# Performance work log

Measured on AMD Instinct MI355X. Metric: run time of the kernel, lower is better.

The kernel has to match this reference:

```python
import jax, jax.numpy as jnp
import numpy as np

B, N, F_IN = 16, 2048, 64   # batch, node_num, input_dim
D = 64                      # dim == embed_dim == GNN out_channel
TOPK = 30
EPS = 1e-5
NEG_SLOPE = 0.2


def setup_inputs() -> dict:
    key = jax.random.key(0)
    k = jax.random.split(key, 20)
    u = lambda kk, shp, b: jax.random.uniform(kk, shp, jnp.float32, -b, b)
    return {
        "data": jax.random.normal(k[0], (B, N, F_IN), jnp.float32),
        "org_edge_index": jax.random.randint(k[1], (2, N * TOPK), 0, N),  # accepted but unused (prior_graph=True)
        "embedding_weight": u(k[2], (N, D), 1.0 / np.sqrt(D)),            # kaiming_uniform(a=sqrt(5)) bound
        "lin_w": u(k[3], (F_IN, D), 1.0 / np.sqrt(F_IN)),
        "att_i": jax.random.normal(k[4], (D,), jnp.float32) * 0.1,
        "att_j": jax.random.normal(k[5], (D,), jnp.float32) * 0.1,
        "att_em_i": jax.random.normal(k[6], (D,), jnp.float32) * 0.1,
        "att_em_j": jax.random.normal(k[7], (D,), jnp.float32) * 0.1,
        "gnn_bias": jax.random.normal(k[8], (D,), jnp.float32) * 0.01,
        "bn1_gamma": jax.random.uniform(k[9], (D,), jnp.float32, 0.5, 1.5),
        "bn1_beta": jax.random.normal(k[10], (D,), jnp.float32) * 0.1,
        "bn1_mean": jax.random.normal(k[11], (D,), jnp.float32) * 0.1,
        "bn1_var": jax.random.uniform(k[12], (D,), jnp.float32, 0.5, 1.5),
        "bn2_gamma": jax.random.uniform(k[13], (D,), jnp.float32, 0.5, 1.5),
        "bn2_beta": jax.random.normal(k[14], (D,), jnp.float32) * 0.1,
        "bn2_mean": jax.random.normal(k[15], (D,), jnp.float32) * 0.1,
        "bn2_var": jax.random.uniform(k[16], (D,), jnp.float32, 0.5, 1.5),
        "out_w": u(k[17], (D, 1), 1.0 / np.sqrt(D)),
        "out_b": jnp.zeros((1,), jnp.float32),
    }


def _forward(data, org_edge_index, embedding_weight, lin_w, att_i, att_j,
             att_em_i, att_em_j, gnn_bias,
             bn1_gamma, bn1_beta, bn1_mean, bn1_var,
             bn2_gamma, bn2_beta, bn2_mean, bn2_var,
             out_w, out_b):
    b, n, f = data.shape
    x = jax.lax.stop_gradient(data).reshape(b * n, f)  # torch: x = data.clone().detach()

    # --- dynamic graph: top-k cosine similarity over DETACHED embeddings ---
    w = jax.lax.stop_gradient(embedding_weight)        # weights_arr = embedding.detach().clone()
    nrm = jnp.linalg.norm(w, axis=-1, keepdims=True)
    cos = (w @ w.T) / (nrm * nrm.T)                    # [N, N]
    _, topk_idx = jax.lax.top_k(cos, TOPK)             # [N, k]; row i contains i itself (cos(i,i)=1 is the max),
                                                       # so remove_self_loops + add_self_loops leaves the edge set unchanged
    # batched sources; target of edge (i, kk) is node i -> each node receives exactly TOPK edges
    src = (topk_idx[None] + (jnp.arange(b) * n)[:, None, None]).reshape(b * n, TOPK)

    # --- GraphLayer (GAT-style, heads=1, concat=False -> mean over 1 head) ---
    xl = x @ lin_w                                     # [BN, D]
    emb_all = jnp.tile(embedding_weight, (b, 1))       # [BN, D] embeddings repeated per batch
    a_i = xl @ att_i + emb_all @ att_em_i              # per-node target score [BN]
    a_j = xl @ att_j + emb_all @ att_em_j              # per-node source score [BN]
    alpha = jax.nn.leaky_relu(a_i[:, None] + a_j[src], NEG_SLOPE)  # [BN, k]
    alpha = jax.nn.softmax(alpha, axis=-1)             # softmax over incoming edges per target node
    out = jnp.einsum('ek,ekd->ed', alpha, xl[src]) + gnn_bias      # per-edge gather + weighted add-aggregate

    # GNNLayer: BatchNorm1d (eval) + ReLU
    out = (out - bn1_mean) / jnp.sqrt(bn1_var + EPS) * bn1_gamma + bn1_beta
    out = jax.nn.relu(out)

    # --- readout ---
    h = out.reshape(b, n, D) * embedding_weight[None]  # elementwise mul with node embeddings
    h = (h - bn2_mean) / jnp.sqrt(bn2_var + EPS) * bn2_gamma + bn2_beta  # bn_outlayer_in (eval)
    h = jax.nn.relu(h)                                 # dropout = identity (eval)
    y = h @ out_w + out_b                              # OutLayer: single Linear(D, 1)
    return y.reshape(-1, n)                            # [B, N]


def reference(data, org_edge_index, embedding_weight, lin_w, att_i, att_j,
              att_em_i, att_em_j, gnn_bias,
              bn1_gamma, bn1_beta, bn1_mean, bn1_var,
              bn2_gamma, bn2_beta, bn2_mean, bn2_var,
              out_w, out_b):
    return _forward(data, org_edge_index, embedding_weight, lin_w, att_i, att_j,
                    att_em_i, att_em_j, gnn_bias,
                    bn1_gamma, bn1_beta, bn1_mean, bn1_var,
                    bn2_gamma, bn2_beta, bn2_mean, bn2_var,
                    out_w, out_b)
```

## Files before the change

kernel.cpp:

```cpp
#include <hip/hip_runtime.h>
#include <hip/hip_bf16.h>

#define NODES 2048
#define DIM   64
#define K_TOP 30
#define BATCH 16
#define BN    (NODES * BATCH)
#define NEGINF (-3.402823466e38f)
#define EPS 1e-5f
#define TB 64

template <int CTRL>
__device__ __forceinline__ float dpp_add_f32(float x) {
    int y = __builtin_amdgcn_update_dpp(0, __float_as_int(x), CTRL, 0xf, 0xf, true);
    return x + __int_as_float(y);
}

__device__ __forceinline__ float wave_sum(float x) {
    x = dpp_add_f32<0x111>(x);
    x = dpp_add_f32<0x112>(x);
    x = dpp_add_f32<0x114>(x);
    x = dpp_add_f32<0x118>(x);
    x = dpp_add_f32<0x142>(x);
    x = dpp_add_f32<0x143>(x);
    return __int_as_float(__builtin_amdgcn_readlane(__float_as_int(x), 63));
}

template <int CTRL>
__device__ __forceinline__ float dpp_max_f32(float x) {
    int y = __builtin_amdgcn_update_dpp(__float_as_int(x), __float_as_int(x),
                                        CTRL, 0xf, 0xf, false);
    return fmaxf(x, __int_as_float(y));
}

__device__ __forceinline__ float wave_max(float x) {
    x = dpp_max_f32<0x111>(x);
    x = dpp_max_f32<0x112>(x);
    x = dpp_max_f32<0x114>(x);
    x = dpp_max_f32<0x118>(x);
    x = dpp_max_f32<0x142>(x);
    x = dpp_max_f32<0x143>(x);
    return __int_as_float(__builtin_amdgcn_readlane(__float_as_int(x), 63));
}

#define ARGMAX_STEP(CTRL)                                                       \
    do {                                                                        \
        int nv_ = __builtin_amdgcn_update_dpp(__float_as_int(bv),               \
                      __float_as_int(bv), (CTRL), 0xf, 0xf, false);             \
        int nj_ = __builtin_amdgcn_update_dpp(bj, bj, (CTRL), 0xf, 0xf, false); \
        float nvf_ = __int_as_float(nv_);                                       \
        bool g_ = (nvf_ > bv) || (nvf_ == bv && nj_ < bj);                      \
        bv = g_ ? nvf_ : bv;                                                    \
        bj = g_ ? nj_ : bj;                                                     \
    } while (0)

#define TOP3_INSERT(x, j)                                                        \
    do {                                                                         \
        if ((x) > m1)      { m3 = m2; j3 = j2; m2 = m1; j2 = j1; m1 = (x); j1 = (j); } \
        else if ((x) > m2) { m3 = m2; j3 = j2; m2 = (x); j2 = (j); }             \
        else if ((x) > m3) { m3 = (x); j3 = (j); }                               \
    } while (0)

__global__ __launch_bounds__(256) void normalize_kernel(const float* __restrict__ w,
                                                        float* __restrict__ wn) {
    int r = blockIdx.x * 4 + (threadIdx.x >> 6);
    int lane = threadIdx.x & 63;
    float v = w[r * DIM + lane];
    float s = wave_sum(v * v);
    wn[r * DIM + lane] = v * rsqrtf(s);
}

__global__ __launch_bounds__(256) void cos_kernel(const float* __restrict__ wn,
                                                  float* __restrict__ cosm) {
    __shared__ float As[TB][DIM + 1];
    __shared__ float Bs[TB][DIM + 1];
    const int tid = threadIdx.x;
    const int bi = blockIdx.x, bj = blockIdx.y;

    for (int s = tid; s < TB * DIM; s += 256) {
        int r = s >> 6, d = s & 63;
        As[r][d] = wn[(bi * TB + r) * DIM + d];
        Bs[r][d] = wn[(bj * TB + r) * DIM + d];
    }
    __syncthreads();

    const int ti = tid >> 4, tj = tid & 15;
    float acc[4][4] = {};
    #pragma unroll 16
    for (int k = 0; k < DIM; ++k) {
        float a[4], b[4];
        #pragma unroll
        for (int u = 0; u < 4; ++u) a[u] = As[ti * 4 + u][k];
        #pragma unroll
        for (int v = 0; v < 4; ++v) b[v] = Bs[tj * 4 + v][k];
        #pragma unroll
        for (int u = 0; u < 4; ++u)
            #pragma unroll
            for (int v = 0; v < 4; ++v)
                acc[u][v] = fmaf(a[u], b[v], acc[u][v]);
    }
    #pragma unroll
    for (int u = 0; u < 4; ++u) {
        float4 o = make_float4(acc[u][0], acc[u][1], acc[u][2], acc[u][3]);
        *(float4*)&cosm[(size_t)(bi * TB + ti * 4 + u) * NODES + bj * TB + tj * 4] = o;
    }
}

__global__ __launch_bounds__(256) void topk_kernel(const float* __restrict__ cosm,
                                                   int* __restrict__ topk) {
    __shared__ float sv[4][NODES / 64][64];
    const int w = threadIdx.x >> 6;
    const int lane = threadIdx.x & 63;
    const int i = blockIdx.x * 4 + w;
    const float* row = cosm + (size_t)i * NODES;

    float m1 = NEGINF, m2 = NEGINF, m3 = NEGINF;
    int j1 = 0, j2 = 0, j3 = 0;
    #pragma unroll
    for (int q = 0; q < NODES / 64; ++q) {
        float x = row[q * 64 + lane];
        sv[w][q][lane] = x;
        TOP3_INSERT(x, q * 64 + lane);
    }
    int live = 3;

    int res = 0;
    #pragma unroll 1
    for (int t = 0; t < K_TOP; ++t) {
        float bv = m1;
        int bj = j1;
        ARGMAX_STEP(0x111);
        ARGMAX_STEP(0x112);
        ARGMAX_STEP(0x114);
        ARGMAX_STEP(0x118);
        ARGMAX_STEP(0x142);
        ARGMAX_STEP(0x143);
        const int wj = __builtin_amdgcn_readlane(bj, 63);
        res = (lane == t) ? wj : res;
        if (lane == (wj & 63)) {
            sv[w][wj >> 6][lane] = NEGINF;
            m1 = m2; j1 = j2; m2 = m3; j2 = j3; m3 = NEGINF;
            if (--live == 0) {
                m1 = m2 = m3 = NEGINF; j1 = j2 = j3 = 0;
                #pragma unroll
                for (int q = 0; q < NODES / 64; ++q) {
                    float x = sv[w][q][lane];
                    TOP3_INSERT(x, q * 64 + lane);
                }
                live = 3;
            }
        }
    }
    if (lane < K_TOP) topk[i * K_TOP + lane] = res;
}

__global__ __launch_bounds__(256) void lin_kernel(const float* __restrict__ x,
                                                  const float* __restrict__ lin_w,
                                                  const float* __restrict__ emb,
                                                  const float* __restrict__ att_i,
                                                  const float* __restrict__ att_j,
                                                  const float* __restrict__ att_em_i,
                                                  const float* __restrict__ att_em_j,
                                                  float* __restrict__ xl,
                                                  float* __restrict__ ai,
                                                  float* __restrict__ aj) {
    __shared__ float lw[DIM * DIM];
    __shared__ float xs[16 * DIM];
    const int tid = threadIdx.x;
    const int wave = tid >> 6;
    const int lane = tid & 63;
    const int row0 = blockIdx.x * 16;

    for (int t = tid; t < DIM * DIM; t += 256) lw[t] = lin_w[t];
    for (int t = tid; t < 16 * DIM; t += 256) xs[t] = x[row0 * DIM + t];
    __syncthreads();

    for (int rr = wave; rr < 16; rr += 4) {
        const int r = row0 + rr;
        float acc = 0.f;
        #pragma unroll
        for (int f = 0; f < DIM; ++f)
            acc = fmaf(xs[rr * DIM + f], lw[f * DIM + lane], acc);
        xl[r * DIM + lane] = acc;

        const int i = r & (NODES - 1);
        const float em = emb[i * DIM + lane];
        float ti = wave_sum(acc * att_i[lane] + em * att_em_i[lane]);
        float tj = wave_sum(acc * att_j[lane] + em * att_em_j[lane]);
        if (lane == 0) { ai[r] = ti; aj[r] = tj; }
    }
}

__global__ __launch_bounds__(256) void agg_kernel(const int* __restrict__ topk,
                                                  const float* __restrict__ xl,
                                                  const float* __restrict__ ai,
                                                  const float* __restrict__ aj,
                                                  const float* __restrict__ emb,
                                                  const float* __restrict__ gnn_bias,
                                                  const float* __restrict__ g1, const float* __restrict__ b1,
                                                  const float* __restrict__ m1, const float* __restrict__ v1,
                                                  const float* __restrict__ g2, const float* __restrict__ b2,
                                                  const float* __restrict__ m2, const float* __restrict__ v2,
                                                  const float* __restrict__ out_w,
                                                  const float* __restrict__ out_b,
                                                  float* __restrict__ y) {
    const int e = blockIdx.x * 4 + (threadIdx.x >> 6);
    const int lane = threadIdx.x & 63;
    const int i = e & (NODES - 1);
    const int b = e >> 11;

    const float a_ie = ai[e];
    int nbr = 0;
    float raw = NEGINF;
    if (lane < K_TOP) {
        nbr = (b << 11) + topk[i * K_TOP + lane];
        float r0 = a_ie + aj[nbr];
        raw = (r0 >= 0.f) ? r0 : 0.2f * r0;
    }
    const float m = wave_max(raw);
    float p = (lane < K_TOP) ? __expf(raw - m) : 0.f;
    const float s = wave_sum(p);
    const float inv = 1.f / s;

    float acc = 0.f;
    #pragma unroll
    for (int k = 0; k < K_TOP; ++k) {
        const float pk = __int_as_float(__builtin_amdgcn_readlane(__float_as_int(p), k));
        const int nb = __builtin_amdgcn_readlane(nbr, k);
        acc = fmaf(pk, xl[nb * DIM + lane], acc);
    }

    float o = acc * inv + gnn_bias[lane];
    o = (o - m1[lane]) * rsqrtf(v1[lane] + EPS) * g1[lane] + b1[lane];
    o = fmaxf(o, 0.f);
    float h = o * emb[i * DIM + lane];
    h = (h - m2[lane]) * rsqrtf(v2[lane] + EPS) * g2[lane] + b2[lane];
    h = fmaxf(h, 0.f);
    float t = wave_sum(h * out_w[lane]);
    if (lane == 0) y[e] = t + out_b[0];
}

extern "C" void kernel_launch(void* const* d_in, const int* in_sizes, int n_in,
                              void* d_out, int out_size, void* d_ws, size_t ws_size,
                              hipStream_t stream) {
    const float* data      = (const float*)d_in[0];
    const float* emb       = (const float*)d_in[2];
    const float* lin_w     = (const float*)d_in[3];
    const float* att_i     = (const float*)d_in[4];
    const float* att_j     = (const float*)d_in[5];
    const float* att_em_i  = (const float*)d_in[6];
    const float* att_em_j  = (const float*)d_in[7];
    const float* gnn_bias  = (const float*)d_in[8];
    const float* bn1_gamma = (const float*)d_in[9];
    const float* bn1_beta  = (const float*)d_in[10];
    const float* bn1_mean  = (const float*)d_in[11];
    const float* bn1_var   = (const float*)d_in[12];
    const float* bn2_gamma = (const float*)d_in[13];
    const float* bn2_beta  = (const float*)d_in[14];
    const float* bn2_mean  = (const float*)d_in[15];
    const float* bn2_var   = (const float*)d_in[16];
    const float* out_w     = (const float*)d_in[17];
    const float* out_b     = (const float*)d_in[18];
    float* y = (float*)d_out;

    char* ws = (char*)d_ws;
    float* cosm = (float*)(ws);
    float* xl   = (float*)(ws);
    float* ai   = (float*)(ws + 8 * 1024 * 1024);
    float* aj   = (float*)(ws + 8 * 1024 * 1024 + 131072);
    float* wn   = (float*)(ws + 16 * 1024 * 1024);
    int*   topk = (int*)  (ws + 16 * 1024 * 1024 + 524288);

    normalize_kernel<<<NODES / 4, 256, 0, stream>>>(emb, wn);
    cos_kernel<<<dim3(NODES / TB, NODES / TB), 256, 0, stream>>>(wn, cosm);
    topk_kernel<<<NODES / 4, 256, 0, stream>>>(cosm, topk);
    lin_kernel<<<BN / 16, 256, 0, stream>>>(data, lin_w, emb, att_i, att_j,
                                            att_em_i, att_em_j, xl, ai, aj);
    agg_kernel<<<BN / 4, 256, 0, stream>>>(topk, xl, ai, aj, emb, gnn_bias,
                                           bn1_gamma, bn1_beta, bn1_mean, bn1_var,
                                           bn2_gamma, bn2_beta, bn2_mean, bn2_var,
                                           out_w, out_b, y);
}
```

Baseline: 176.9 us.

## Enlarge cosine-similarity tiles to 128x128 with transposed shared memory and 8x8 microtiles

The cosine similarity GEMM now uses 128x128 block tiles and 8x8 per-thread register tiles. Shared memory is stored transposed with padding so operands are read as float4 vectors. This raises arithmetic intensity per shared load and reduces block count. In exchange it brings higher register pressure, fewer blocks (one per CU), and possible bank conflicts on the transposed stores.

Result: no change. 175.7 us (-0.7%).

```diff
diff --git a/kernel.cpp b/kernel.cpp
--- a/kernel.cpp
+++ b/kernel.cpp
@@ -8,7 +8,8 @@
 #define BN    (NODES * BATCH)
 #define NEGINF (-3.402823466e38f)
 #define EPS 1e-5f
-#define TB 64
+#define TBC 128
+#define KPAD 132
 
 template <int CTRL>
 __device__ __forceinline__ float dpp_add_f32(float x) {
@@ -70,39 +71,44 @@
     wn[r * DIM + lane] = v * rsqrtf(s);
 }
 
-__global__ __launch_bounds__(256) void cos_kernel(const float* __restrict__ wn,
-                                                  float* __restrict__ cosm) {
-    __shared__ float As[TB][DIM + 1];
-    __shared__ float Bs[TB][DIM + 1];
+__global__ __launch_bounds__(256, 1) void cos_kernel(const float* __restrict__ wn,
+                                                     float* __restrict__ cosm) {
+    __shared__ float AsT[DIM][KPAD];
+    __shared__ float BsT[DIM][KPAD];
     const int tid = threadIdx.x;
     const int bi = blockIdx.x, bj = blockIdx.y;
 
-    for (int s = tid; s < TB * DIM; s += 256) {
+    #pragma unroll
+    for (int it = 0; it < 32; ++it) {
+        int s = it * 256 + tid;
         int r = s >> 6, d = s & 63;
-        As[r][d] = wn[(bi * TB + r) * DIM + d];
-        Bs[r][d] = wn[(bj * TB + r) * DIM + d];
+        AsT[d][r] = wn[(bi * TBC + r) * DIM + d];
+        BsT[d][r] = wn[(bj * TBC + r) * DIM + d];
     }
     __syncthreads();
 
-    const int ti = tid >> 4, tj = tid & 15;
-    float acc[4][4] = {};
-    #pragma unroll 16
+    const int ti = tid >> 4;
+    const int tj = tid & 15;
+    float acc[8][8] = {};
+    #pragma unroll 4
     for (int k = 0; k < DIM; ++k) {
-        float a[4], b[4];
+        float4 a0 = *(const float4*)&AsT[k][ti * 8];
+        float4 a1 = *(const float4*)&AsT[k][ti * 8 + 4];
+        float4 b0 = *(const float4*)&BsT[k][tj * 8];
+        float4 b1 = *(const float4*)&BsT[k][tj * 8 + 4];
+        float a[8] = {a0.x, a0.y, a0.z, a0.w, a1.x, a1.y, a1.z, a1.w};
+        float b[8] = {b0.x, b0.y, b0.z, b0.w, b1.x, b1.y, b1.z, b1.w};
         #pragma unroll
-        for (int u = 0; u < 4; ++u) a[u] = As[ti * 4 + u][k];
-        #pragma unroll
-        for (int v = 0; v < 4; ++v) b[v] = Bs[tj * 4 + v][k];
-        #pragma unroll
-        for (int u = 0; u < 4; ++u)
+        for (int u = 0; u < 8; ++u)
             #pragma unroll
-            for (int v = 0; v < 4; ++v)
+            for (int v = 0; v < 8; ++v)
                 acc[u][v] = fmaf(a[u], b[v], acc[u][v]);
     }
     #pragma unroll
-    for (int u = 0; u < 4; ++u) {
-        float4 o = make_float4(acc[u][0], acc[u][1], acc[u][2], acc[u][3]);
-        *(float4*)&cosm[(size_t)(bi * TB + ti * 4 + u) * NODES + bj * TB + tj * 4] = o;
+    for (int u = 0; u < 8; ++u) {
+        const size_t base = (size_t)(bi * TBC + ti * 8 + u) * NODES + bj * TBC + tj * 8;
+        *(float4*)&cosm[base]     = make_float4(acc[u][0], acc[u][1], acc[u][2], acc[u][3]);
+        *(float4*)&cosm[base + 4] = make_float4(acc[u][4], acc[u][5], acc[u][6], acc[u][7]);
     }
 }
 
@@ -272,7 +278,7 @@
     int*   topk = (int*)  (ws + 16 * 1024 * 1024 + 524288);
 
     normalize_kernel<<<NODES / 4, 256, 0, stream>>>(emb, wn);
-    cos_kernel<<<dim3(NODES / TB, NODES / TB), 256, 0, stream>>>(wn, cosm);
+    cos_kernel<<<dim3(NODES / TBC, NODES / TBC), 256, 0, stream>>>(wn, cosm);
     topk_kernel<<<NODES / 4, 256, 0, stream>>>(cosm, topk);
     lin_kernel<<<BN / 16, 256, 0, stream>>>(data, lin_w, emb, att_i, att_j,
                                             att_em_i, att_em_j, xl, ai, aj);
```
